# Kernel tuning notes

Measured on AMD Instinct MI355X. Metric: run time of the kernel, lower is better.

The kernel has to match this reference:

```python
import jax, jax.numpy as jnp
import numpy as np

D_MODEL = 1024
N_HEADS = 16
D_K = D_MODEL // N_HEADS


def setup_inputs() -> dict:
    key = jax.random.key(0)
    ks = jax.random.split(key, 6)
    B, S = 4, 2048
    x = jax.random.normal(ks[0], (B, S, D_MODEL), dtype=jnp.float32)
    # nn.Linear weights are [out, in]; kept in that layout, applied as x @ W.T
    lim = 1.0 / np.sqrt(D_MODEL)
    w_q = jax.random.uniform(ks[1], (D_MODEL, D_MODEL), jnp.float32, -lim, lim)
    w_k = jax.random.uniform(ks[2], (D_MODEL, D_MODEL), jnp.float32, -lim, lim)
    w_v = jax.random.uniform(ks[3], (D_MODEL, D_MODEL), jnp.float32, -lim, lim)
    w_o = jax.random.uniform(ks[4], (D_MODEL, D_MODEL), jnp.float32, -lim, lim)
    b_o = jax.random.uniform(ks[5], (D_MODEL,), jnp.float32, -lim, lim)
    return {"x": x, "w_q": w_q, "w_k": w_k, "w_v": w_v, "w_o": w_o, "b_o": b_o}


def reference(x, w_q, w_k, w_v, w_o, b_o):
    B, S, _ = x.shape
    scale = 1.0 / np.sqrt(D_K).astype(np.float32)

    def split_heads(t):  # [B,S,D] -> [B,H,S,d_k]
        return t.reshape(B, S, N_HEADS, D_K).transpose(0, 2, 1, 3)

    q = split_heads(x @ w_q.T)
    k = split_heads(x @ w_k.T)
    v = split_heads(x @ w_v.T)

    scores = jnp.einsum('bhqd,bhkd->bhqk', q, k) * scale
    causal = jnp.tril(jnp.ones((S, S), dtype=bool))
    scores = jnp.where(causal[None, None], scores, -jnp.inf)
    attn = jax.nn.softmax(scores, axis=-1)  # dropout p=0 -> identity
    out = jnp.einsum('bhqk,bhkd->bhqd', attn, v)
    out = out.transpose(0, 2, 1, 3).reshape(B, S, D_MODEL)
    return out @ w_o.T + b_o
```

## Files before the change

kernel.cpp:

```cpp
#include <hip/hip_runtime.h>

typedef unsigned short ushort_t;
typedef __attribute__((ext_vector_type(8))) short short8;
typedef __attribute__((ext_vector_type(4))) float floatx4;


__device__ __forceinline__ ushort_t f2bf(float f) {
    unsigned int u = __float_as_uint(f);
    u = (u + 0x7FFFu + ((u >> 16) & 1u)) >> 16;
    return (ushort_t)u;
}

typedef __attribute__((address_space(1))) void gls_g;
typedef __attribute__((address_space(3))) void gls_l;

__device__ __forceinline__ void async_copy16(const ushort_t* g, ushort_t* l) {
    __builtin_amdgcn_global_load_lds((gls_g*)g, (gls_l*)l, 16, 0, 0);
}

__device__ __forceinline__ floatx4 mfma16(short8 a, short8 b, floatx4 c) {
    return __builtin_amdgcn_mfma_f32_16x16x32_bf16(a, b, c, 0, 0, 0);
}


__global__ __launch_bounds__(256) void conv_all(const float* __restrict__ x,
                                                const float* __restrict__ wq,
                                                const float* __restrict__ wk,
                                                const float* __restrict__ wv,
                                                const float* __restrict__ wo,
                                                ushort_t* __restrict__ xb,
                                                ushort_t* __restrict__ wqkv,
                                                ushort_t* __restrict__ wob) {
    const int bid = blockIdx.x;
    const float* in;
    ushort_t* out;
    int blk;
    if (bid < 8192) { in = x; out = xb; blk = bid; }
    else {
        const int g = (bid - 8192) >> 10;
        blk = (bid - 8192) & 1023;
        in  = (g == 0) ? wq : (g == 1) ? wk : (g == 2) ? wv : wo;
        out = (g == 3) ? wob : wqkv + g * 1048576;
    }
    const int i = (blk * 256 + threadIdx.x) * 4;
    float4 f = *(const float4*)(in + i);
    ushort4 o;
    o.x = f2bf(f.x); o.y = f2bf(f.y); o.z = f2bf(f.z); o.w = f2bf(f.w);
    *(ushort4*)(out + i) = o;
}


template<int MODE>
__global__ __launch_bounds__(256, 2) void gemm_nt(const ushort_t* __restrict__ A,
                                                  const ushort_t* __restrict__ B,
                                                  void* __restrict__ Cv,
                                                  const float* __restrict__ bias,
                                                  int M, int N, int K, int ldc,
                                                  ushort_t* __restrict__ vt) {
    __shared__ ushort_t lA[128 * 64];
    __shared__ ushort_t lB[128 * 64];
    const int tid  = threadIdx.x;
    const int wave = tid >> 6, lane = tid & 63;
    const int quad = lane >> 4, l15 = lane & 15;
    const int wr = (wave >> 1) * 64;
    const int wc = (wave & 1) * 64;
    const size_t bm = blockIdx.y, bn = blockIdx.x;

    const ushort_t* Ab = A + bm * 128 * (size_t)K;
    const ushort_t* Bb = B + bn * 128 * (size_t)K;

    int srow[4], scol[4];
#pragma unroll
    for (int i = 0; i < 4; ++i) {
        const int li = i * 256 + tid;
        srow[i] = li >> 3;
        scol[i] = ((li & 7) ^ (srow[i] & 7)) * 8;
    }

    floatx4 acc[4][4];
#pragma unroll
    for (int i = 0; i < 4; ++i)
#pragma unroll
        for (int j = 0; j < 4; ++j) acc[i][j] = (floatx4){0.f, 0.f, 0.f, 0.f};

    for (int kt = 0; kt < K; kt += 64) {
        __syncthreads();
#pragma unroll
        for (int i = 0; i < 4; ++i) {
            async_copy16(Ab + (size_t)srow[i] * K + kt + scol[i],
                         &lA[i * 2048] + wave * 512);
            async_copy16(Bb + (size_t)srow[i] * K + kt + scol[i],
                         &lB[i * 2048] + wave * 512);
        }
        __syncthreads();

        short8 af[4][2], bf[4][2];
#pragma unroll
        for (int mt = 0; mt < 4; ++mt)
#pragma unroll
            for (int ks = 0; ks < 2; ++ks)
                af[mt][ks] = *(const short8*)&lA[(wr + mt * 16 + l15) * 64 +
                                                 (((ks * 4 + quad) ^ (l15 & 7)) * 8)];
#pragma unroll
        for (int nt = 0; nt < 4; ++nt)
#pragma unroll
            for (int ks = 0; ks < 2; ++ks)
                bf[nt][ks] = *(const short8*)&lB[(wc + nt * 16 + l15) * 64 +
                                                 (((ks * 4 + quad) ^ (l15 & 7)) * 8)];
#pragma unroll
        for (int mt = 0; mt < 4; ++mt)
#pragma unroll
            for (int nt = 0; nt < 4; ++nt) {
                acc[mt][nt] = mfma16(af[mt][0], bf[nt][0], acc[mt][nt]);
                acc[mt][nt] = mfma16(af[mt][1], bf[nt][1], acc[mt][nt]);
            }
    }

    if (MODE == 0) {
#pragma unroll
        for (int mt = 0; mt < 4; ++mt)
#pragma unroll
            for (int nt = 0; nt < 4; ++nt)
#pragma unroll
                for (int r = 0; r < 4; ++r) {
                    const size_t m = bm * 128 + wr + mt * 16 + quad * 4 + r;
                    const size_t n = bn * 128 + wc + nt * 16 + l15;
                    ((float*)Cv)[m * (size_t)ldc + n] = acc[mt][nt][r] + bias[n];
                }
    } else if ((int)bn < 16) {
#pragma unroll
        for (int mt = 0; mt < 4; ++mt)
#pragma unroll
            for (int nt = 0; nt < 4; ++nt)
#pragma unroll
                for (int r = 0; r < 4; ++r) {
                    const size_t m = bm * 128 + wr + mt * 16 + quad * 4 + r;
                    const size_t n = bn * 128 + wc + nt * 16 + l15;
                    ((ushort_t*)Cv)[m * (size_t)ldc + n] = f2bf(acc[mt][nt][r]);
                }
    } else {
        const int hh = ((int)bn - 16) * 2 + (wc >> 6);
        const int bb = (int)(bm >> 4);
        const size_t srow_off = (bm & 15) * 128 + wr;
#pragma unroll
        for (int mt = 0; mt < 4; ++mt)
#pragma unroll
            for (int nt = 0; nt < 4; ++nt) {
                ushort4 ov;
                ov.x = f2bf(acc[mt][nt][0]);
                ov.y = f2bf(acc[mt][nt][1]);
                ov.z = f2bf(acc[mt][nt][2]);
                ov.w = f2bf(acc[mt][nt][3]);
                ushort_t* dst = vt +
                    ((size_t)((bb * 16 + hh) * 64 + nt * 16 + l15)) * 2048 +
                    srow_off + (mt >> 1) * 32 + (mt & 1) * 4 + quad * 8;
                *(ushort4*)dst = ov;
            }
    }
}


__device__ __forceinline__ short8 score_group(const short8 (&kg)[2][2],
                                              short8 qf0, short8 qf1,
                                              int dmask, int mt,
                                              int quad, int l15, float& lacc) {
    const float C = 0.18033688011112042f;
    const floatx4 z = {0.f, 0.f, 0.f, 0.f};
    float p[8];
    floatx4 s0 = mfma16(kg[0][0], qf0, z);
    s0 = mfma16(kg[0][1], qf1, s0);
    if (dmask && mt == 0) {
#pragma unroll
        for (int r = 0; r < 4; ++r) {
            p[r] = __builtin_amdgcn_exp2f(s0[r] * C);
            if (quad * 4 + r > l15) p[r] = 0.f;
            p[r + 4] = 0.f;
        }
    } else {
        floatx4 s1 = mfma16(kg[1][0], qf0, z);
        s1 = mfma16(kg[1][1], qf1, s1);
#pragma unroll
        for (int r = 0; r < 4; ++r) {
            p[r]     = __builtin_amdgcn_exp2f(s0[r] * C);
            p[r + 4] = __builtin_amdgcn_exp2f(s1[r] * C);
        }
        if (dmask) {
#pragma unroll
            for (int r = 0; r < 4; ++r)
                if (quad * 4 + r > l15) p[r + 4] = 0.f;
        }
    }
    lacc += ((p[0] + p[1]) + (p[2] + p[3])) + ((p[4] + p[5]) + (p[6] + p[7]));
    union { unsigned u[4]; short8 s8; } pk;
#pragma unroll
    for (int j = 0; j < 4; ++j)
        pk.u[j] = __builtin_amdgcn_perm(__float_as_uint(p[2 * j + 1]),
                                        __float_as_uint(p[2 * j]), 0x07060302u);
    return pk.s8;
}

__global__ __launch_bounds__(256, 2) void attn_fwd(const ushort_t* __restrict__ qkv,
                                                   const ushort_t* __restrict__ vt,
                                                   ushort_t* __restrict__ attn) {
    __shared__ ushort_t lK[2][4096];
    __shared__ ushort_t lV[2][4096];
    const int tid = threadIdx.x, wave = tid >> 6, lane = tid & 63;
    const int quad = lane >> 4, l15 = lane & 15;
    const int bh = blockIdx.x & 63;
    const int ord = blockIdx.x >> 6;
    const int b = bh >> 4, h = bh & 15;

    const ushort_t* qb = qkv + (size_t)b * 2048 * 3072 + h * 64;
    const ushort_t* kb = qb + 1024;
    const ushort_t* vb = vt + (size_t)(bh * 64) * 2048;

    const int r0 = tid >> 3;
    const int r1 = 32 + r0;
    const int c0 = ((tid & 7) ^ (r0 & 7)) * 8;
    const int kc0 = (quad ^ (l15 & 7)) * 8;
    const int kc1 = ((4 + quad) ^ (l15 & 7)) * 8;

    const int phase = (ord < 8) ? 1 : 0;
    const int slot  = (ord < 8) ? ord : 15 - ord;
    const int t = phase ? 63 - (slot * 4 + wave) : slot * 4 + wave;
    const int tmaxb = phase ? 63 - slot * 4 : slot * 4 + 3;
    const int n64 = (tmaxb >> 1) + 1;
    const int Td = t >> 1;
    const int todd = t & 1;
    const int q0 = t * 32;

    short8 qf[2][2];
#pragma unroll
    for (int mt = 0; mt < 2; ++mt)
#pragma unroll
        for (int ks = 0; ks < 2; ++ks)
            qf[mt][ks] = *(const short8*)(qb +
                (size_t)(q0 + mt * 16 + l15) * 3072 + ks * 32 + quad * 8);

    floatx4 o[2][4];
    float l[2] = {0.f, 0.f};
#pragma unroll
    for (int mt = 0; mt < 2; ++mt)
#pragma unroll
        for (int d = 0; d < 4; ++d) o[mt][d] = (floatx4){0.f, 0.f, 0.f, 0.f};

    async_copy16(kb + (size_t)r0 * 3072 + c0, &lK[0][0]    + wave * 512);
    async_copy16(kb + (size_t)r1 * 3072 + c0, &lK[0][2048] + wave * 512);
    async_copy16(vb + (size_t)r0 * 2048 + c0, &lV[0][0]    + wave * 512);
    async_copy16(vb + (size_t)r1 * 2048 + c0, &lV[0][2048] + wave * 512);

#pragma unroll 1
    for (int T = 0; T < n64; ++T) {
        __syncthreads();
        if (T + 1 < n64) {
            const int nb = (T + 1) & 1;
            const ushort_t* kn = kb + (size_t)(T + 1) * 196608;
            const ushort_t* vn = vb + (T + 1) * 64;
            async_copy16(kn + (size_t)r0 * 3072 + c0, &lK[nb][0]    + wave * 512);
            async_copy16(kn + (size_t)r1 * 3072 + c0, &lK[nb][2048] + wave * 512);
            async_copy16(vn + (size_t)r0 * 2048 + c0, &lV[nb][0]    + wave * 512);
            async_copy16(vn + (size_t)r1 * 2048 + c0, &lV[nb][2048] + wave * 512);
        }
        if (T <= Td) {
            const int buf = T & 1;
            const ushort_t* Kb = &lK[buf][0];
            const ushort_t* Vb = &lV[buf][0];
            const bool diagT = (T == Td);
            const bool hasG1 = (T < Td) || todd;
            const int g0m = (diagT && !todd) ? 1 : 0;
            const int g1m = (diagT && todd) ? 1 : 0;

            short8 k0[2][2], v0[4], k1[2][2], v1[4];
#pragma unroll
            for (int s = 0; s < 2; ++s) {
                k0[s][0] = *(const short8*)(Kb + (s * 16 + l15) * 64 + kc0);
                k0[s][1] = *(const short8*)(Kb + (s * 16 + l15) * 64 + kc1);
            }
#pragma unroll
            for (int d = 0; d < 4; ++d)
                v0[d] = *(const short8*)(Vb + (d * 16 + l15) * 64 + kc0);
            if (hasG1) {
#pragma unroll
                for (int s = 0; s < 2; ++s) {
                    k1[s][0] = *(const short8*)(Kb + ((2 + s) * 16 + l15) * 64 + kc0);
                    k1[s][1] = *(const short8*)(Kb + ((2 + s) * 16 + l15) * 64 + kc1);
                }
#pragma unroll
                for (int d = 0; d < 4; ++d)
                    v1[d] = *(const short8*)(Vb + (d * 16 + l15) * 64 + kc1);
            }

#pragma unroll
            for (int mt = 0; mt < 2; ++mt) {
                const short8 pb0 = score_group(k0, qf[mt][0], qf[mt][1],
                                               g0m, mt, quad, l15, l[mt]);
#pragma unroll
                for (int d = 0; d < 4; ++d)
                    o[mt][d] = mfma16(v0[d], pb0, o[mt][d]);
                if (hasG1) {
                    const short8 pb1 = score_group(k1, qf[mt][0], qf[mt][1],
                                                   g1m, mt, quad, l15, l[mt]);
#pragma unroll
                    for (int d = 0; d < 4; ++d)
                        o[mt][d] = mfma16(v1[d], pb1, o[mt][d]);
                }
            }
        }
    }

#pragma unroll
    for (int mt = 0; mt < 2; ++mt) {
        float lt = l[mt];
        lt += __shfl_xor(lt, 16);
        lt += __shfl_xor(lt, 32);
        const float inv = 1.0f / lt;
        ushort_t* orow = attn + (size_t)(b * 2048 + q0 + mt * 16 + l15) * 1024 + h * 64;
#pragma unroll
        for (int d = 0; d < 4; ++d) {
            ushort4 ov;
            ov.x = f2bf(o[mt][d][0] * inv);
            ov.y = f2bf(o[mt][d][1] * inv);
            ov.z = f2bf(o[mt][d][2] * inv);
            ov.w = f2bf(o[mt][d][3] * inv);
            *(ushort4*)(orow + d * 16 + quad * 4) = ov;
        }
    }
}


extern "C" void kernel_launch(void* const* d_in, const int* in_sizes, int n_in,
                              void* d_out, int out_size, void* d_ws, size_t ws_size,
                              hipStream_t stream) {
    const float* x  = (const float*)d_in[0];
    const float* wq = (const float*)d_in[1];
    const float* wk = (const float*)d_in[2];
    const float* wv = (const float*)d_in[3];
    const float* wo = (const float*)d_in[4];
    const float* bo = (const float*)d_in[5];

    char* ws = (char*)d_ws;
    ushort_t* xb   = (ushort_t*)(ws);
    ushort_t* wqkv = (ushort_t*)(ws + 16777216);
    ushort_t* wob  = (ushort_t*)(ws + 23068672);
    ushort_t* qkv  = (ushort_t*)(ws + 25165824);
    ushort_t* vtb  = (ushort_t*)(ws + 75497472);
    ushort_t* attn = xb;
    float* out = (float*)d_out;

    conv_all<<<12288, 256, 0, stream>>>(x, wq, wk, wv, wo, xb, wqkv, wob);

    gemm_nt<1><<<dim3(24, 64), 256, 0, stream>>>(xb, wqkv, qkv, nullptr,
                                                 8192, 3072, 1024, 3072, vtb);
    attn_fwd<<<1024, 256, 0, stream>>>(qkv, vtb, attn);
    gemm_nt<0><<<dim3(8, 64), 256, 0, stream>>>(attn, wob, out, bo,
                                                8192, 1024, 1024, 1024, nullptr);
}
```

Before: 225.0 us.

## Add dedicated 128x256 triple-buffered QKV GEMM kernel with 8 waves

```diff
diff --git a/kernel.cpp b/kernel.cpp
--- a/kernel.cpp
+++ b/kernel.cpp
@@ -127,21 +127,120 @@
                     const size_t n = bn * 128 + wc + nt * 16 + l15;
                     ((float*)Cv)[m * (size_t)ldc + n] = acc[mt][nt][r] + bias[n];
                 }
-    } else if ((int)bn < 16) {
+    }
+}
+
+
+__global__ __launch_bounds__(512, 2) void gemm8_qkv(const ushort_t* __restrict__ A,
+                                                    const ushort_t* __restrict__ B,
+                                                    ushort_t* __restrict__ Cq,
+                                                    ushort_t* __restrict__ vt) {
+    __shared__ __attribute__((aligned(16))) ushort_t lA[3][128 * 64];
+    __shared__ __attribute__((aligned(16))) ushort_t lB[3][256 * 64];
+    const int tid  = threadIdx.x;
+    const int wave = tid >> 6, lane = tid & 63;
+    const int quad = lane >> 4, l15 = lane & 15;
+    const int wm = wave >> 2, wn = wave & 3;
+
+    const int swz = (blockIdx.x & 7) * 96 + (blockIdx.x >> 3);
+    const int bm = swz / 12, bn = swz % 12;
+
+    const ushort_t* Ab = A + (size_t)bm * 128 * 1024;
+    const ushort_t* Bb = B + (size_t)bn * 256 * 1024;
+
+    int arow[2], acol[2], brow[4], bcol[4];
+#pragma unroll
+    for (int i = 0; i < 2; ++i) {
+        const int li = i * 512 + tid;
+        arow[i] = li >> 3; acol[i] = ((li & 7) ^ (arow[i] & 7)) * 8;
+    }
+#pragma unroll
+    for (int i = 0; i < 4; ++i) {
+        const int li = i * 512 + tid;
+        brow[i] = li >> 3; bcol[i] = ((li & 7) ^ (brow[i] & 7)) * 8;
+    }
+
+    floatx4 acc[4][4];
+#pragma unroll
+    for (int i = 0; i < 4; ++i)
+#pragma unroll
+        for (int j = 0; j < 4; ++j) acc[i][j] = (floatx4){0.f, 0.f, 0.f, 0.f};
+
+    auto issue = [&](int t, int buf) {
+        const int kt = t * 64;
+#pragma unroll
+        for (int i = 0; i < 2; ++i)
+            async_copy16(Ab + (size_t)arow[i] * 1024 + kt + acol[i],
+                         &lA[buf][i * 4096] + wave * 512);
+#pragma unroll
+        for (int i = 0; i < 4; ++i)
+            async_copy16(Bb + (size_t)brow[i] * 1024 + kt + bcol[i],
+                         &lB[buf][i * 4096] + wave * 512);
+    };
+
+    auto step = [&](int buf) {
+        const ushort_t* La = &lA[buf][0];
+        const ushort_t* Lb = &lB[buf][0];
+        short8 af[4][2], bfr[4][2];
+#pragma unroll
+        for (int mt = 0; mt < 4; ++mt)
+#pragma unroll
+            for (int ks = 0; ks < 2; ++ks)
+                af[mt][ks] = *(const short8*)&La[(wm * 64 + mt * 16 + l15) * 64 +
+                                                (((ks * 4 + quad) ^ (l15 & 7)) * 8)];
+#pragma unroll
+        for (int nt = 0; nt < 4; ++nt)
+#pragma unroll
+            for (int ks = 0; ks < 2; ++ks)
+                bfr[nt][ks] = *(const short8*)&Lb[(wn * 64 + nt * 16 + l15) * 64 +
+                                                 (((ks * 4 + quad) ^ (l15 & 7)) * 8)];
+        __builtin_amdgcn_s_setprio(1);
+#pragma unroll
+        for (int mt = 0; mt < 4; ++mt)
+#pragma unroll
+            for (int nt = 0; nt < 4; ++nt) {
+                acc[mt][nt] = mfma16(af[mt][0], bfr[nt][0], acc[mt][nt]);
+                acc[mt][nt] = mfma16(af[mt][1], bfr[nt][1], acc[mt][nt]);
+            }
+        __builtin_amdgcn_s_setprio(0);
+    };
+
+    issue(0, 0);
+    issue(1, 1);
+    asm volatile("s_waitcnt vmcnt(6)" ::: "memory");
+    __builtin_amdgcn_sched_barrier(0);
+    __builtin_amdgcn_s_barrier();
+
+#pragma unroll 1
+    for (int t = 0; t < 14; ++t) {
+        issue(t + 2, (t + 2) % 3);
+        step(t % 3);
+        asm volatile("s_waitcnt vmcnt(6)" ::: "memory");
+        __builtin_amdgcn_sched_barrier(0);
+        __builtin_amdgcn_s_barrier();
+    }
+    step(2);
+    asm volatile("s_waitcnt vmcnt(0)" ::: "memory");
+    __builtin_amdgcn_sched_barrier(0);
+    __builtin_amdgcn_s_barrier();
+    step(0);
+
+    const int mrow0 = bm * 128 + wm * 64;
+    if (bn < 8) {
 #pragma unroll
         for (int mt = 0; mt < 4; ++mt)
 #pragma unroll
             for (int nt = 0; nt < 4; ++nt)
 #pragma unroll
                 for (int r = 0; r < 4; ++r) {
-                    const size_t m = bm * 128 + wr + mt * 16 + quad * 4 + r;
-                    const size_t n = bn * 128 + wc + nt * 16 + l15;
-                    ((ushort_t*)Cv)[m * (size_t)ldc + n] = f2bf(acc[mt][nt][r]);
+                    const size_t m = mrow0 + mt * 16 + quad * 4 + r;
+                    const size_t n = bn * 256 + wn * 64 + nt * 16 + l15;
+                    Cq[m * 3072 + n] = f2bf(acc[mt][nt][r]);
                 }
     } else {
-        const int hh = ((int)bn - 16) * 2 + (wc >> 6);
-        const int bb = (int)(bm >> 4);
-        const size_t srow_off = (bm & 15) * 128 + wr;
+        const int hh = (bn - 8) * 4 + wn;
+        const int bb = bm >> 4;
+        const size_t srow_off = (bm & 15) * 128 + wm * 64;
 #pragma unroll
         for (int mt = 0; mt < 4; ++mt)
 #pragma unroll
@@ -349,8 +448,7 @@
 
     conv_all<<<12288, 256, 0, stream>>>(x, wq, wk, wv, wo, xb, wqkv, wob);
 
-    gemm_nt<1><<<dim3(24, 64), 256, 0, stream>>>(xb, wqkv, qkv, nullptr,
-                                                 8192, 3072, 1024, 3072, vtb);
+    gemm8_qkv<<<768, 512, 0, stream>>>(xb, wqkv, qkv, vtb);
     attn_fwd<<<1024, 256, 0, stream>>>(qkv, vtb, attn);
     gemm_nt<0><<<dim3(8, 64), 256, 0, stream>>>(attn, wob, out, bo,
                                                 8192, 1024, 1024, 1024, nullptr);
```

Result: slower. 241.8 us (+7.5%).
